# Kernel optimization log

Hardware: AMD Instinct MI355X
Metric: run time of the kernel (lower is better)

The kernel has to match this reference:

```python
import jax, jax.numpy as jnp
import numpy as np

GOP = 4

def _resize_bilinear(x, Ho, Wo):
    # x: (M, C, Hs, Ws); matches F.interpolate(mode='bilinear', align_corners=False)
    M, C, Hs, Ws = x.shape
    ys = jnp.clip((jnp.arange(Ho, dtype=jnp.float32) + 0.5) * (Hs / Ho) - 0.5, 0.0, Hs - 1.0)
    xs = jnp.clip((jnp.arange(Wo, dtype=jnp.float32) + 0.5) * (Ws / Wo) - 0.5, 0.0, Ws - 1.0)
    y0 = jnp.floor(ys).astype(jnp.int32); y1 = jnp.minimum(y0 + 1, Hs - 1)
    x0 = jnp.floor(xs).astype(jnp.int32); x1 = jnp.minimum(x0 + 1, Ws - 1)
    wy = (ys - y0)[None, None, :, None]
    wx = (xs - x0)[None, None, None, :]
    r0 = x[:, :, y0, :]; r1 = x[:, :, y1, :]
    top = r0[:, :, :, x0] * (1 - wx) + r0[:, :, :, x1] * wx
    bot = r1[:, :, :, x0] * (1 - wx) + r1[:, :, :, x1] * wx
    return top * (1 - wy) + bot * wy

def _deform_sample(feat, flow):
    # feat: (M,C,H,W); flow: (M,2,H,W), ch0=dy, ch1=dx (torchvision deform_conv order).
    # Bilinear sample at (y+dy, x+dx) with zero padding outside (kernel_size=1 deform conv).
    M, C, H, W = feat.shape
    gy = jnp.arange(H, dtype=flow.dtype)[:, None]
    gx = jnp.arange(W, dtype=flow.dtype)[None, :]
    y = gy + flow[:, 0]; x = gx + flow[:, 1]          # (M,H,W)
    y0f = jnp.floor(y); x0f = jnp.floor(x)
    wy = (y - y0f)[:, None]; wx = (x - x0f)[:, None]  # (M,1,H,W)
    y0 = y0f.astype(jnp.int32); x0 = x0f.astype(jnp.int32)
    feat_flat = feat.reshape(M, C, H * W)
    def gather(yi, xi):
        valid = ((yi >= 0) & (yi < H) & (xi >= 0) & (xi < W)).astype(feat.dtype)
        idx = (jnp.clip(yi, 0, H - 1) * W + jnp.clip(xi, 0, W - 1)).reshape(M, H * W)
        v = jnp.take_along_axis(feat_flat, jnp.broadcast_to(idx[:, None, :], (M, C, H * W)), axis=2)
        return v.reshape(M, C, H, W) * valid[:, None]
    v00 = gather(y0, x0);     v01 = gather(y0, x0 + 1)
    v10 = gather(y0 + 1, x0); v11 = gather(y0 + 1, x0 + 1)
    return v00 * (1 - wy) * (1 - wx) + v01 * (1 - wy) * wx + v10 * wy * (1 - wx) + v11 * wy * wx

def setup_inputs():
    key = jax.random.key(0)
    k = jax.random.split(key, 7)
    B, T, Himg, Wimg = 4, 16, 256, 256
    num_gop = T // GOP      # 4
    t = GOP - 1             # 3 P-frames per GOP
    C_in, D, h, w = 256, 256, 64, 64
    imgs = jnp.zeros((B, T, 3, Himg, Wimg), jnp.float32)
    i_features = jax.random.normal(k[0], (B * num_gop, C_in, h, w), jnp.float32)
    # flows of a few pixels at image scale (scaled by 0.25 inside forward)
    p_motions = jax.random.normal(k[1], (B, num_gop * t, 2, Himg, Wimg), jnp.float32) * 8.0
    W_emb = jax.random.normal(k[2], (D, C_in), jnp.float32) * 0.02
    b_emb = jax.random.normal(k[3], (D,), jnp.float32) * 0.02
    W_dc = jax.random.normal(k[4], (D, D), jnp.float32) * 0.02
    b_dc = jax.random.normal(k[5], (D,), jnp.float32) * 0.02
    return {"imgs": imgs, "i_features": i_features, "p_motions": p_motions,
            "W_emb": W_emb, "b_emb": b_emb, "W_dc": W_dc, "b_dc": b_dc}

def reference(imgs, i_features, p_motions, W_emb, b_emb, W_dc, b_dc):
    B = imgs.shape[0]
    num_gop = imgs.shape[1] // GOP
    # 1x1 embedding conv
    feat = jnp.einsum('mchw,oc->mohw', i_features, W_emb) + b_emb[None, :, None, None]
    M0, D, h, w = feat.shape
    scale = w / imgs.shape[-1]
    Tp = p_motions.shape[1]
    flow = _resize_bilinear(p_motions.reshape(B * Tp, 2, p_motions.shape[-2], p_motions.shape[-1]), h, w) * scale
    t = Tp // num_gop
    # repeat each GOP's I-frame features for its t P-frame flows
    feat = jnp.broadcast_to(feat.reshape(B, num_gop, 1, D, h, w), (B, num_gop, t, D, h, w)).reshape(-1, D, h, w)
    flow = flow.reshape(-1, 2, h, w)
    # flow-guided deformable conv with 1x1 kernel: bilinear gather + 1x1 projection
    samp = _deform_sample(feat, flow)
    out = jnp.einsum('mchw,oc->mohw', samp, W_dc) + b_dc[None, :, None, None]
    # adaptive_avg_pool2d(.,1).flatten(3)
    return out.mean(axis=(-2, -1)).reshape(B, num_gop, t, D)
```

## Files before the change

### kernel.cpp

```cpp
#include <hip/hip_runtime.h>
#include <math.h>

#define HW 4096
#define CIN 256
#define DD 256
#define M_TOTAL 48
#define NSP 4
#define SPPX (HW / NSP)

__global__ __launch_bounds__(256) void k_pre(
    const float* __restrict__ p_motions,
    const float* __restrict__ W_emb,
    const float* __restrict__ b_emb,
    const float* __restrict__ W_dc,
    float* __restrict__ Ag4,
    float* __restrict__ Sg4,
    float* __restrict__ WT,
    float* __restrict__ bfold,
    float* __restrict__ out)
{
    const int tid = threadIdx.x;
    const int bid = blockIdx.x;

    if (bid < M_TOTAL * NSP) {
        __shared__ float Al[HW];
        __shared__ float red[4];
        const int m = bid >> 2;
        const int sp = bid & 3;
        const float4* p0 = (const float4*)(p_motions + (size_t)m * 2 * 65536);
        const float4* p1 = p0 + 65536 / 4;

        for (int i = tid; i < HW; i += 256) Al[i] = 0.f;
        __syncthreads();

        #pragma unroll
        for (int ii = 0; ii < SPPX / 256; ++ii) {
            const int i = ii * 256 + tid;
            const int y = sp * 16 + (i >> 6);
            const int x = i & 63;
            const int r1 = 4 * y + 1, r2 = 4 * y + 2;
            const float4 v10 = p0[r1 * 64 + x];
            const float4 v20 = p0[r2 * 64 + x];
            const float4 v11 = p1[r1 * 64 + x];
            const float4 v21 = p1[r2 * 64 + x];
            const float fy = (v10.y + v10.z + v20.y + v20.z) * 0.0625f;
            const float fx = (v11.y + v11.z + v21.y + v21.z) * 0.0625f;

            const float yy = (float)y + fy;
            const float xx = (float)x + fx;
            const float y0f = floorf(yy), x0f = floorf(xx);
            const float wy = yy - y0f, wx = xx - x0f;
            const int iy0 = (int)y0f, ix0 = (int)x0f;
            const int iy1 = iy0 + 1, ix1 = ix0 + 1;
            const float w00 = (1.f - wy) * (1.f - wx);
            const float w01 = (1.f - wy) * wx;
            const float w10 = wy * (1.f - wx);
            const float w11 = wy * wx;
            const bool y0ok = (iy0 >= 0) & (iy0 < 64);
            const bool y1ok = (iy1 >= 0) & (iy1 < 64);
            const bool x0ok = (ix0 >= 0) & (ix0 < 64);
            const bool x1ok = (ix1 >= 0) & (ix1 < 64);
            if (y0ok & x0ok) atomicAdd(&Al[iy0 * 64 + ix0], w00);
            if (y0ok & x1ok) atomicAdd(&Al[iy0 * 64 + ix1], w01);
            if (y1ok & x0ok) atomicAdd(&Al[iy1 * 64 + ix0], w10);
            if (y1ok & x1ok) atomicAdd(&Al[iy1 * 64 + ix1], w11);
        }
        __syncthreads();

        const float4* Al4 = (const float4*)Al;
        float4* dst = (float4*)(Ag4 + (size_t)(m * NSP + sp) * HW);
        float part = 0.f;
        #pragma unroll
        for (int i = tid; i < HW / 4; i += 256) {
            const float4 v = Al4[i];
            dst[i] = v;
            part += v.x + v.y + v.z + v.w;
        }
        for (int off = 32; off > 0; off >>= 1) part += __shfl_down(part, off, 64);
        if ((tid & 63) == 0) red[tid >> 6] = part;
        __syncthreads();
        if (tid == 0) Sg4[m * NSP + sp] = red[0] + red[1] + red[2] + red[3];
    } else {
        __shared__ float wdc[256];
        __shared__ float red2[4];
        const int o = bid - M_TOTAL * NSP;
        wdc[tid] = W_dc[(size_t)o * 256 + tid];
        if (tid < 48) out[(size_t)o * 48 + tid] = 0.f;
        __syncthreads();
        float acc = 0.f;
        #pragma unroll 8
        for (int k = 0; k < 256; ++k)
            acc += wdc[k] * W_emb[(size_t)k * 256 + tid];
        WT[(size_t)tid * 256 + o] = acc;

        float pb = wdc[tid] * b_emb[tid];
        for (int off = 32; off > 0; off >>= 1) pb += __shfl_down(pb, off, 64);
        if ((tid & 63) == 0) red2[tid >> 6] = pb;
        __syncthreads();
        if (tid == 0) bfold[o] = red2[0] + red2[1] + red2[2] + red2[3];
    }
}

__global__ __launch_bounds__(256, 4) void k_gather_out(
    const float* __restrict__ i_features,
    const float* __restrict__ Ag4,
    const float* __restrict__ Sg4,
    const float* __restrict__ WT,
    const float* __restrict__ bfold,
    const float* __restrict__ b_dc,
    float* __restrict__ out)
{
    __shared__ float gl[3][16];
    const int fm = blockIdx.x;
    const int chunk = blockIdx.y;
    const int sp = blockIdx.z;
    const int tid = threadIdx.x;
    const int wave = tid >> 6, lane = tid & 63;
    const int m0 = fm * 3;

    float4 a[3][4];
    #pragma unroll
    for (int j = 0; j < 3; ++j) {
        const float4* P0 = (const float4*)(Ag4 + ((size_t)((m0 + j) * NSP + 0)) * HW + sp * SPPX);
        const float4* P1 = (const float4*)(Ag4 + ((size_t)((m0 + j) * NSP + 1)) * HW + sp * SPPX);
        const float4* P2 = (const float4*)(Ag4 + ((size_t)((m0 + j) * NSP + 2)) * HW + sp * SPPX);
        const float4* P3 = (const float4*)(Ag4 + ((size_t)((m0 + j) * NSP + 3)) * HW + sp * SPPX);
        #pragma unroll
        for (int k = 0; k < 4; ++k) {
            const float4 t0 = P0[lane + 64 * k];
            const float4 t1 = P1[lane + 64 * k];
            const float4 t2 = P2[lane + 64 * k];
            const float4 t3 = P3[lane + 64 * k];
            a[j][k].x = t0.x + t1.x + t2.x + t3.x;
            a[j][k].y = t0.y + t1.y + t2.y + t3.y;
            a[j][k].z = t0.z + t1.z + t2.z + t3.z;
            a[j][k].w = t0.w + t1.w + t2.w + t3.w;
        }
    }

    #pragma unroll
    for (int c = 0; c < 4; ++c) {
        const int ci = chunk * 16 + wave * 4 + c;
        const float4* f4 = (const float4*)(i_features + ((size_t)fm * CIN + ci) * HW + sp * SPPX);
        float s0 = 0.f, s1 = 0.f, s2 = 0.f;
        #pragma unroll
        for (int k = 0; k < 4; ++k) {
            const float4 v = f4[lane + 64 * k];
            s0 += v.x * a[0][k].x + v.y * a[0][k].y + v.z * a[0][k].z + v.w * a[0][k].w;
            s1 += v.x * a[1][k].x + v.y * a[1][k].y + v.z * a[1][k].z + v.w * a[1][k].w;
            s2 += v.x * a[2][k].x + v.y * a[2][k].y + v.z * a[2][k].z + v.w * a[2][k].w;
        }
        #pragma unroll
        for (int off = 32; off > 0; off >>= 1) {
            s0 += __shfl_down(s0, off, 64);
            s1 += __shfl_down(s1, off, 64);
            s2 += __shfl_down(s2, off, 64);
        }
        if (lane == 0) {
            gl[0][wave * 4 + c] = s0;
            gl[1][wave * 4 + c] = s1;
            gl[2][wave * 4 + c] = s2;
        }
    }
    __syncthreads();

    const int o = tid;
    float acc0 = 0.f, acc1 = 0.f, acc2 = 0.f;
    #pragma unroll
    for (int q = 0; q < 16; ++q) {
        const float wv = WT[(size_t)(chunk * 16 + q) * DD + o];
        acc0 += gl[0][q] * wv;
        acc1 += gl[1][q] * wv;
        acc2 += gl[2][q] * wv;
    }
    const float inv = 1.f / 4096.f;
    atomicAdd(&out[(size_t)(m0 + 0) * DD + o], acc0 * inv);
    atomicAdd(&out[(size_t)(m0 + 1) * DD + o], acc1 * inv);
    atomicAdd(&out[(size_t)(m0 + 2) * DD + o], acc2 * inv);

    if (chunk == 0 && sp == 0) {
        #pragma unroll
        for (int j = 0; j < 3; ++j) {
            const int m = m0 + j;
            const float Sm = (Sg4[m * NSP + 0] + Sg4[m * NSP + 1] +
                              Sg4[m * NSP + 2] + Sg4[m * NSP + 3]) * inv;
            atomicAdd(&out[(size_t)m * DD + tid], bfold[tid] * Sm + b_dc[tid]);
        }
    }
}

extern "C" void kernel_launch(void* const* d_in, const int* in_sizes, int n_in,
                              void* d_out, int out_size, void* d_ws, size_t ws_size,
                              hipStream_t stream) {
    const float* i_features = (const float*)d_in[1];
    const float* p_motions  = (const float*)d_in[2];
    const float* W_emb      = (const float*)d_in[3];
    const float* b_emb      = (const float*)d_in[4];
    const float* W_dc       = (const float*)d_in[5];
    const float* b_dc       = (const float*)d_in[6];
    float* out = (float*)d_out;

    float* ws = (float*)d_ws;
    float* Ag4   = ws;
    float* Sg4   = Ag4 + (size_t)M_TOTAL * NSP * HW;
    float* WT    = Sg4 + 256;
    float* bfold = WT + 65536;

    k_pre<<<M_TOTAL * NSP + DD, 256, 0, stream>>>(p_motions, W_emb, b_emb, W_dc,
                                                  Ag4, Sg4, WT, bfold, out);
    dim3 g2(16, 16, NSP);
    k_gather_out<<<g2, 256, 0, stream>>>(i_features, Ag4, Sg4, WT, bfold, b_dc, out);
}
```

Measured before the change: 157.4 us.

## Fuse pre-pass and gather into one cooperative kernel with grid sync

New measurement: 249.3 us. 58.4% more time.

```diff
diff --git a/kernel.cpp b/kernel.cpp
--- a/kernel.cpp
+++ b/kernel.cpp
@@ -1,4 +1,5 @@
 #include <hip/hip_runtime.h>
+#include <hip/hip_cooperative_groups.h>
 #include <math.h>
 
 #define HW 4096
@@ -8,123 +9,107 @@
 #define NSP 4
 #define SPPX (HW / NSP)
 
-__global__ __launch_bounds__(256) void k_pre(
-    const float* __restrict__ p_motions,
-    const float* __restrict__ W_emb,
-    const float* __restrict__ b_emb,
-    const float* __restrict__ W_dc,
-    float* __restrict__ Ag4,
-    float* __restrict__ Sg4,
-    float* __restrict__ WT,
-    float* __restrict__ bfold,
-    float* __restrict__ out)
-{
-    const int tid = threadIdx.x;
-    const int bid = blockIdx.x;
-
-    if (bid < M_TOTAL * NSP) {
-        __shared__ float Al[HW];
-        __shared__ float red[4];
-        const int m = bid >> 2;
-        const int sp = bid & 3;
-        const float4* p0 = (const float4*)(p_motions + (size_t)m * 2 * 65536);
-        const float4* p1 = p0 + 65536 / 4;
-
-        for (int i = tid; i < HW; i += 256) Al[i] = 0.f;
-        __syncthreads();
-
-        #pragma unroll
-        for (int ii = 0; ii < SPPX / 256; ++ii) {
-            const int i = ii * 256 + tid;
-            const int y = sp * 16 + (i >> 6);
-            const int x = i & 63;
-            const int r1 = 4 * y + 1, r2 = 4 * y + 2;
-            const float4 v10 = p0[r1 * 64 + x];
-            const float4 v20 = p0[r2 * 64 + x];
-            const float4 v11 = p1[r1 * 64 + x];
-            const float4 v21 = p1[r2 * 64 + x];
-            const float fy = (v10.y + v10.z + v20.y + v20.z) * 0.0625f;
-            const float fx = (v11.y + v11.z + v21.y + v21.z) * 0.0625f;
-
-            const float yy = (float)y + fy;
-            const float xx = (float)x + fx;
-            const float y0f = floorf(yy), x0f = floorf(xx);
-            const float wy = yy - y0f, wx = xx - x0f;
-            const int iy0 = (int)y0f, ix0 = (int)x0f;
-            const int iy1 = iy0 + 1, ix1 = ix0 + 1;
-            const float w00 = (1.f - wy) * (1.f - wx);
-            const float w01 = (1.f - wy) * wx;
-            const float w10 = wy * (1.f - wx);
-            const float w11 = wy * wx;
-            const bool y0ok = (iy0 >= 0) & (iy0 < 64);
-            const bool y1ok = (iy1 >= 0) & (iy1 < 64);
-            const bool x0ok = (ix0 >= 0) & (ix0 < 64);
-            const bool x1ok = (ix1 >= 0) & (ix1 < 64);
-            if (y0ok & x0ok) atomicAdd(&Al[iy0 * 64 + ix0], w00);
-            if (y0ok & x1ok) atomicAdd(&Al[iy0 * 64 + ix1], w01);
-            if (y1ok & x0ok) atomicAdd(&Al[iy1 * 64 + ix0], w10);
-            if (y1ok & x1ok) atomicAdd(&Al[iy1 * 64 + ix1], w11);
-        }
-        __syncthreads();
-
-        const float4* Al4 = (const float4*)Al;
-        float4* dst = (float4*)(Ag4 + (size_t)(m * NSP + sp) * HW);
-        float part = 0.f;
-        #pragma unroll
-        for (int i = tid; i < HW / 4; i += 256) {
-            const float4 v = Al4[i];
-            dst[i] = v;
-            part += v.x + v.y + v.z + v.w;
-        }
-        for (int off = 32; off > 0; off >>= 1) part += __shfl_down(part, off, 64);
-        if ((tid & 63) == 0) red[tid >> 6] = part;
-        __syncthreads();
-        if (tid == 0) Sg4[m * NSP + sp] = red[0] + red[1] + red[2] + red[3];
-    } else {
-        __shared__ float wdc[256];
-        __shared__ float red2[4];
-        const int o = bid - M_TOTAL * NSP;
-        wdc[tid] = W_dc[(size_t)o * 256 + tid];
-        if (tid < 48) out[(size_t)o * 48 + tid] = 0.f;
-        __syncthreads();
-        float acc = 0.f;
-        #pragma unroll 8
-        for (int k = 0; k < 256; ++k)
-            acc += wdc[k] * W_emb[(size_t)k * 256 + tid];
-        WT[(size_t)tid * 256 + o] = acc;
-
-        float pb = wdc[tid] * b_emb[tid];
-        for (int off = 32; off > 0; off >>= 1) pb += __shfl_down(pb, off, 64);
-        if ((tid & 63) == 0) red2[tid >> 6] = pb;
-        __syncthreads();
-        if (tid == 0) bfold[o] = red2[0] + red2[1] + red2[2] + red2[3];
-    }
-}
-
-__global__ __launch_bounds__(256, 4) void k_gather_out(
-    const float* __restrict__ i_features,
-    const float* __restrict__ Ag4,
-    const float* __restrict__ Sg4,
-    const float* __restrict__ WT,
-    const float* __restrict__ bfold,
-    const float* __restrict__ b_dc,
-    float* __restrict__ out)
-{
-    __shared__ float gl[3][16];
-    const int fm = blockIdx.x;
-    const int chunk = blockIdx.y;
-    const int sp = blockIdx.z;
-    const int tid = threadIdx.x;
-    const int wave = tid >> 6, lane = tid & 63;
-    const int m0 = fm * 3;
+namespace cg = cooperative_groups;
+
+__device__ __forceinline__ void scatter_block(
+    const float* __restrict__ p_motions, float* __restrict__ Ag4,
+    float* __restrict__ Sg4, float* Al, float* red, int m, int sp, int tid)
+{
+    const float4* p0 = (const float4*)(p_motions + (size_t)m * 2 * 65536);
+    const float4* p1 = p0 + 65536 / 4;
+
+    for (int i = tid; i < HW; i += 256) Al[i] = 0.f;
+    __syncthreads();
+
+    #pragma unroll
+    for (int ii = 0; ii < SPPX / 256; ++ii) {
+        const int i = ii * 256 + tid;
+        const int y = sp * 16 + (i >> 6);
+        const int x = i & 63;
+        const int r1 = 4 * y + 1, r2 = 4 * y + 2;
+        const float4 v10 = p0[r1 * 64 + x];
+        const float4 v20 = p0[r2 * 64 + x];
+        const float4 v11 = p1[r1 * 64 + x];
+        const float4 v21 = p1[r2 * 64 + x];
+        const float fy = (v10.y + v10.z + v20.y + v20.z) * 0.0625f;
+        const float fx = (v11.y + v11.z + v21.y + v21.z) * 0.0625f;
+
+        const float yy = (float)y + fy;
+        const float xx = (float)x + fx;
+        const float y0f = floorf(yy), x0f = floorf(xx);
+        const float wy = yy - y0f, wx = xx - x0f;
+        const int iy0 = (int)y0f, ix0 = (int)x0f;
+        const int iy1 = iy0 + 1, ix1 = ix0 + 1;
+        const float w00 = (1.f - wy) * (1.f - wx);
+        const float w01 = (1.f - wy) * wx;
+        const float w10 = wy * (1.f - wx);
+        const float w11 = wy * wx;
+        const bool y0ok = (iy0 >= 0) & (iy0 < 64);
+        const bool y1ok = (iy1 >= 0) & (iy1 < 64);
+        const bool x0ok = (ix0 >= 0) & (ix0 < 64);
+        const bool x1ok = (ix1 >= 0) & (ix1 < 64);
+        if (y0ok & x0ok) atomicAdd(&Al[iy0 * 64 + ix0], w00);
+        if (y0ok & x1ok) atomicAdd(&Al[iy0 * 64 + ix1], w01);
+        if (y1ok & x0ok) atomicAdd(&Al[iy1 * 64 + ix0], w10);
+        if (y1ok & x1ok) atomicAdd(&Al[iy1 * 64 + ix1], w11);
+    }
+    __syncthreads();
+
+    const float4* Al4 = (const float4*)Al;
+    float4* dst = (float4*)(Ag4 + (size_t)(m * NSP + sp) * HW);
+    float part = 0.f;
+    #pragma unroll
+    for (int i = tid; i < HW / 4; i += 256) {
+        const float4 v = Al4[i];
+        dst[i] = v;
+        part += v.x + v.y + v.z + v.w;
+    }
+    for (int off = 32; off > 0; off >>= 1) part += __shfl_down(part, off, 64);
+    if ((tid & 63) == 0) red[tid >> 6] = part;
+    __syncthreads();
+    if (tid == 0) Sg4[m * NSP + sp] = red[0] + red[1] + red[2] + red[3];
+}
+
+__device__ __forceinline__ void fold_block(
+    const float* __restrict__ W_emb, const float* __restrict__ b_emb,
+    const float* __restrict__ W_dc, float* __restrict__ WT,
+    float* __restrict__ bfold, float* __restrict__ out,
+    float* Al, float* red, int o, int tid)
+{
+    Al[tid] = W_dc[(size_t)o * 256 + tid];
+    if (tid < 48) out[(size_t)o * 48 + tid] = 0.f;
+    __syncthreads();
+    float acc = 0.f;
+    #pragma unroll 8
+    for (int k = 0; k < 256; ++k)
+        acc += Al[k] * W_emb[(size_t)k * 256 + tid];
+    WT[(size_t)tid * 256 + o] = acc;
+
+    float pb = Al[tid] * b_emb[tid];
+    for (int off = 32; off > 0; off >>= 1) pb += __shfl_down(pb, off, 64);
+    if ((tid & 63) == 0) red[tid >> 6] = pb;
+    __syncthreads();
+    if (tid == 0) bfold[o] = red[0] + red[1] + red[2] + red[3];
+}
+
+__device__ __forceinline__ void gather_unit(
+    const float* __restrict__ i_features, const float* __restrict__ Ag4,
+    const float* __restrict__ Sg4, const float* __restrict__ WT,
+    const float* __restrict__ bfold, const float* __restrict__ b_dc,
+    float* __restrict__ out, float* gl, int u, int tid, int wave, int lane)
+{
+    const int gfm = u >> 6;
+    const int gchunk = (u >> 2) & 15;
+    const int gsp = u & 3;
+    const int gm0 = gfm * 3;
 
     float4 a[3][4];
     #pragma unroll
     for (int j = 0; j < 3; ++j) {
-        const float4* P0 = (const float4*)(Ag4 + ((size_t)((m0 + j) * NSP + 0)) * HW + sp * SPPX);
-        const float4* P1 = (const float4*)(Ag4 + ((size_t)((m0 + j) * NSP + 1)) * HW + sp * SPPX);
-        const float4* P2 = (const float4*)(Ag4 + ((size_t)((m0 + j) * NSP + 2)) * HW + sp * SPPX);
-        const float4* P3 = (const float4*)(Ag4 + ((size_t)((m0 + j) * NSP + 3)) * HW + sp * SPPX);
+        const float4* P0 = (const float4*)(Ag4 + ((size_t)((gm0 + j) * NSP + 0)) * HW + gsp * SPPX);
+        const float4* P1 = (const float4*)(Ag4 + ((size_t)((gm0 + j) * NSP + 1)) * HW + gsp * SPPX);
+        const float4* P2 = (const float4*)(Ag4 + ((size_t)((gm0 + j) * NSP + 2)) * HW + gsp * SPPX);
+        const float4* P3 = (const float4*)(Ag4 + ((size_t)((gm0 + j) * NSP + 3)) * HW + gsp * SPPX);
         #pragma unroll
         for (int k = 0; k < 4; ++k) {
             const float4 t0 = P0[lane + 64 * k];
@@ -140,8 +125,8 @@
 
     #pragma unroll
     for (int c = 0; c < 4; ++c) {
-        const int ci = chunk * 16 + wave * 4 + c;
-        const float4* f4 = (const float4*)(i_features + ((size_t)fm * CIN + ci) * HW + sp * SPPX);
+        const int ci = gchunk * 16 + wave * 4 + c;
+        const float4* f4 = (const float4*)(i_features + ((size_t)gfm * CIN + ci) * HW + gsp * SPPX);
         float s0 = 0.f, s1 = 0.f, s2 = 0.f;
         #pragma unroll
         for (int k = 0; k < 4; ++k) {
@@ -157,9 +142,9 @@
             s2 += __shfl_down(s2, off, 64);
         }
         if (lane == 0) {
-            gl[0][wave * 4 + c] = s0;
-            gl[1][wave * 4 + c] = s1;
-            gl[2][wave * 4 + c] = s2;
+            gl[0 * 16 + wave * 4 + c] = s0;
+            gl[1 * 16 + wave * 4 + c] = s1;
+            gl[2 * 16 + wave * 4 + c] = s2;
         }
     }
     __syncthreads();
@@ -168,25 +153,97 @@
     float acc0 = 0.f, acc1 = 0.f, acc2 = 0.f;
     #pragma unroll
     for (int q = 0; q < 16; ++q) {
-        const float wv = WT[(size_t)(chunk * 16 + q) * DD + o];
-        acc0 += gl[0][q] * wv;
-        acc1 += gl[1][q] * wv;
-        acc2 += gl[2][q] * wv;
+        const float wv = WT[(size_t)(gchunk * 16 + q) * DD + o];
+        acc0 += gl[0 * 16 + q] * wv;
+        acc1 += gl[1 * 16 + q] * wv;
+        acc2 += gl[2 * 16 + q] * wv;
     }
     const float inv = 1.f / 4096.f;
-    atomicAdd(&out[(size_t)(m0 + 0) * DD + o], acc0 * inv);
-    atomicAdd(&out[(size_t)(m0 + 1) * DD + o], acc1 * inv);
-    atomicAdd(&out[(size_t)(m0 + 2) * DD + o], acc2 * inv);
-
-    if (chunk == 0 && sp == 0) {
+    atomicAdd(&out[(size_t)(gm0 + 0) * DD + o], acc0 * inv);
+    atomicAdd(&out[(size_t)(gm0 + 1) * DD + o], acc1 * inv);
+    atomicAdd(&out[(size_t)(gm0 + 2) * DD + o], acc2 * inv);
+
+    if (gchunk == 0 && gsp == 0) {
         #pragma unroll
         for (int j = 0; j < 3; ++j) {
-            const int m = m0 + j;
+            const int m = gm0 + j;
             const float Sm = (Sg4[m * NSP + 0] + Sg4[m * NSP + 1] +
                               Sg4[m * NSP + 2] + Sg4[m * NSP + 3]) * inv;
             atomicAdd(&out[(size_t)m * DD + tid], bfold[tid] * Sm + b_dc[tid]);
         }
     }
+}
+
+__global__ __launch_bounds__(256, 4) void k_fused(
+    const float* __restrict__ i_features,
+    const float* __restrict__ p_motions,
+    const float* __restrict__ W_emb,
+    const float* __restrict__ b_emb,
+    const float* __restrict__ W_dc,
+    const float* __restrict__ b_dc,
+    float* __restrict__ Ag4, float* __restrict__ Sg4,
+    float* __restrict__ WT, float* __restrict__ bfold,
+    float* __restrict__ out)
+{
+    __shared__ float Al[HW];
+    __shared__ float red[4];
+    const int tid = threadIdx.x;
+    const int bid = blockIdx.x;
+    const int wave = tid >> 6, lane = tid & 63;
+
+    if (bid < M_TOTAL * NSP) {
+        scatter_block(p_motions, Ag4, Sg4, Al, red, bid >> 2, bid & 3, tid);
+    } else if (bid < M_TOTAL * NSP + DD) {
+        fold_block(W_emb, b_emb, W_dc, WT, bfold, out, Al, red,
+                   bid - M_TOTAL * NSP, tid);
+    }
+
+    cg::this_grid().sync();
+
+    #pragma unroll
+    for (int r = 0; r < 2; ++r) {
+        const int u = bid + r * 512;
+        gather_unit(i_features, Ag4, Sg4, WT, bfold, b_dc, out,
+                    Al, u, tid, wave, lane);
+        __syncthreads();
+    }
+}
+
+__global__ __launch_bounds__(256) void k_pre(
+    const float* __restrict__ p_motions,
+    const float* __restrict__ W_emb,
+    const float* __restrict__ b_emb,
+    const float* __restrict__ W_dc,
+    float* __restrict__ Ag4, float* __restrict__ Sg4,
+    float* __restrict__ WT, float* __restrict__ bfold,
+    float* __restrict__ out)
+{
+    __shared__ float Al[HW];
+    __shared__ float red[4];
+    const int tid = threadIdx.x;
+    const int bid = blockIdx.x;
+    if (bid < M_TOTAL * NSP)
+        scatter_block(p_motions, Ag4, Sg4, Al, red, bid >> 2, bid & 3, tid);
+    else
+        fold_block(W_emb, b_emb, W_dc, WT, bfold, out, Al, red,
+                   bid - M_TOTAL * NSP, tid);
+}
+
+__global__ __launch_bounds__(256, 4) void k_gather_out(
+    const float* __restrict__ i_features,
+    const float* __restrict__ Ag4,
+    const float* __restrict__ Sg4,
+    const float* __restrict__ WT,
+    const float* __restrict__ bfold,
+    const float* __restrict__ b_dc,
+    float* __restrict__ out)
+{
+    __shared__ float gl[48];
+    const int tid = threadIdx.x;
+    const int wave = tid >> 6, lane = tid & 63;
+    const int u = (blockIdx.x << 6) | (blockIdx.y << 2) | blockIdx.z;
+    gather_unit(i_features, Ag4, Sg4, WT, bfold, b_dc, out,
+                gl, u, tid, wave, lane);
 }
 
 extern "C" void kernel_launch(void* const* d_in, const int* in_sizes, int n_in,
@@ -206,8 +263,20 @@
     float* WT    = Sg4 + 256;
     float* bfold = WT + 65536;
 
-    k_pre<<<M_TOTAL * NSP + DD, 256, 0, stream>>>(p_motions, W_emb, b_emb, W_dc,
-                                                  Ag4, Sg4, WT, bfold, out);
-    dim3 g2(16, 16, NSP);
-    k_gather_out<<<g2, 256, 0, stream>>>(i_features, Ag4, Sg4, WT, bfold, b_dc, out);
-}
+    void* args[] = {
+        (void*)&i_features, (void*)&p_motions, (void*)&W_emb, (void*)&b_emb,
+        (void*)&W_dc, (void*)&b_dc,
+        (void*)&Ag4, (void*)&Sg4, (void*)&WT, (void*)&bfold, (void*)&out
+    };
+    hipError_t e = hipLaunchCooperativeKernel((const void*)k_fused,
+                                              dim3(512), dim3(256),
+                                              args, 0, stream);
+    if (e != hipSuccess) {
+        (void)hipGetLastError();
+        k_pre<<<M_TOTAL * NSP + DD, 256, 0, stream>>>(
+            p_motions, W_emb, b_emb, W_dc, Ag4, Sg4, WT, bfold, out);
+        dim3 g2(16, 16, NSP);
+        k_gather_out<<<g2, 256, 0, stream>>>(
+            i_features, Ag4, Sg4, WT, bfold, b_dc, out);
+    }
+}
```
